# Optimization experiments

Hardware: AMD Instinct MI355X
Metric: run time of the kernel (lower is better)

The kernel has to match this reference:

```python
import jax, jax.numpy as jnp
import numpy as np

COMMITMENT_COST = 0.25


def setup_inputs() -> dict:
    key = jax.random.key(0)
    k1, k2 = jax.random.split(key)
    inputs = jax.random.normal(k1, (16, 1024, 256), dtype=jnp.float32)
    embeddings = jax.random.normal(k2, (8192, 256), dtype=jnp.float32) * 0.1
    return {"inputs": inputs, "embeddings": embeddings}


def reference(inputs, embeddings):
    K, D = embeddings.shape
    input_shape = inputs.shape
    flat = inputs.reshape(-1, D)  # [N, D]
    distances = (
        jnp.sum(flat * flat, axis=1, keepdims=True)
        + jnp.sum(embeddings * embeddings, axis=1)
        - 2.0 * jnp.matmul(flat, embeddings.T)
    )
    encoding_indices = jnp.argmin(distances, axis=1)  # [N]
    # direct codebook gather (same math as one-hot @ embeddings)
    quantized = embeddings[encoding_indices].reshape(input_shape)
    quantized_sg = inputs + jax.lax.stop_gradient(quantized - inputs)
    e_latent_loss = jnp.mean((jax.lax.stop_gradient(quantized) - inputs) ** 2)
    q_latent_loss = jnp.mean((quantized_sg - jax.lax.stop_gradient(quantized)) ** 2)
    loss = q_latent_loss + COMMITMENT_COST * e_latent_loss
    # avg one-hot probabilities = normalized codeword counts
    N = flat.shape[0]
    counts = jnp.zeros((K,), dtype=flat.dtype).at[encoding_indices].add(1.0)
    avg_probs = counts / N
    perplexity = jnp.exp(-jnp.sum(avg_probs * jnp.log(avg_probs + 1e-10)))
    return quantized_sg, encoding_indices, loss, perplexity
```

## Files before the change

### kernel.cpp

```cpp
#include <hip/hip_runtime.h>
#include <math.h>
#include <stdint.h>

#define ND_ROWS 16384
#define DDIM    256
#define KCODES  8192
#define NSEG    128
#define NRG     8

typedef _Float16 f16x4 __attribute__((ext_vector_type(4)));
typedef _Float16 f16x8 __attribute__((ext_vector_type(8)));
typedef float    f32x4v __attribute__((ext_vector_type(4)));
typedef float    f32x16 __attribute__((ext_vector_type(16)));


__device__ __attribute__((always_inline)) inline void load_lds16(const void* g, void* l) {
    __builtin_amdgcn_global_load_lds((const __attribute__((address_space(1))) void*)g,
                                     (__attribute__((address_space(3))) void*)l, 16, 0, 0);
}

__global__ __launch_bounds__(256) void prep_kernel(const float* __restrict__ x,
                                                   const float* __restrict__ emb,
                                                   _Float16* __restrict__ Xp,
                                                   _Float16* __restrict__ Bp,
                                                   float* __restrict__ neF) {
    int wave = (blockIdx.x << 2) + (threadIdx.x >> 6);
    int lane = threadIdx.x & 63;
    if (wave < ND_ROWS) {
        const float* src = x + (size_t)wave * DDIM;
        float4 v = ((const float4*)src)[lane];
        f16x4 hi, lo;
        hi[0] = (_Float16)v.x; lo[0] = (_Float16)(v.x - (float)hi[0]);
        hi[1] = (_Float16)v.y; lo[1] = (_Float16)(v.y - (float)hi[1]);
        hi[2] = (_Float16)v.z; lo[2] = (_Float16)(v.z - (float)hi[2]);
        hi[3] = (_Float16)v.w; lo[3] = (_Float16)(v.w - (float)hi[3]);
        int rb = wave >> 5, rl = wave & 31;
        size_t off = (size_t)rb * 16384 + ((lane >> 2) << 9)
                   + (((lane >> 1) & 1) << 8) + (rl << 3) + ((lane & 1) << 2);
        *(f16x4*)(Xp + off)        = hi;
        *(f16x4*)(Xp + off + 8192) = lo;
    } else {
        int r = wave - ND_ROWS;
        const float* src = emb + (size_t)r * DDIM;
        float4 v = ((const float4*)src)[lane];
        float s = v.x*v.x + v.y*v.y + v.z*v.z + v.w*v.w;
        #pragma unroll
        for (int m = 32; m; m >>= 1) s += __shfl_xor(s, m, 64);
        float4 t;
        t.x = -2.0f * v.x; t.y = -2.0f * v.y; t.z = -2.0f * v.z; t.w = -2.0f * v.w;
        f16x4 hi, lo;
        hi[0] = (_Float16)t.x; lo[0] = (_Float16)(t.x - (float)hi[0]);
        hi[1] = (_Float16)t.y; lo[1] = (_Float16)(t.y - (float)hi[1]);
        hi[2] = (_Float16)t.z; lo[2] = (_Float16)(t.z - (float)hi[2]);
        hi[3] = (_Float16)t.w; lo[3] = (_Float16)(t.w - (float)hi[3]);
        _Float16* dst = Bp + (size_t)r * 512;
        *(f16x4*)(dst + lane * 4)       = hi;
        *(f16x4*)(dst + 256 + lane * 4) = lo;
        if (lane == 0) neF[r] = s;
    }
}

__global__ __launch_bounds__(512, 4) void argmin_seg(
    const _Float16* __restrict__ Xp, const _Float16* __restrict__ Bp,
    const float* __restrict__ neF, unsigned long long* __restrict__ minpair) {
    __shared__ __align__(16) _Float16 Cs[64 * 512];

    const int tid  = threadIdx.x;
    const int lane = tid & 63;
    const int w    = tid >> 6;
    const int c32  = lane & 31;
    const int kg   = lane >> 5;

    const int rg      = blockIdx.x & 7;
    const int seg     = blockIdx.x >> 3;
    const int rowBase = rg * 2048;
    const int code0   = seg * 64;

    #pragma unroll
    for (int i = 0; i < 8; ++i) {
        int cl = w * 8 + i;
        int g  = lane ^ (cl & 7);
        load_lds16((const char*)(Bp + (size_t)(code0 + cl) * 512) + g * 16,
                   (char*)Cs + cl * 1024);
    }
    __syncthreads();

    const int wBase = rowBase + w * 256;
    for (int c2 = 0; c2 < 4; ++c2) {
        const int rb0 = (wBase >> 5) + c2 * 2;
        const char* xb0 = (const char*)Xp + (size_t)rb0 * 32768 + lane * 16;
        const char* xb1 = xb0 + 32768;
        f32x16 acc[2][2];
        #pragma unroll
        for (int i = 0; i < 16; ++i) {
            acc[0][0][i] = 0.0f; acc[0][1][i] = 0.0f;
            acc[1][0][i] = 0.0f; acc[1][1][i] = 0.0f;
        }

        #pragma unroll 2
        for (int q = 0; q < 16; ++q) {
            f16x8 xh0 = *(const f16x8*)(xb0 + q * 1024);
            f16x8 xl0 = *(const f16x8*)(xb0 + 16384 + q * 1024);
            f16x8 xh1 = *(const f16x8*)(xb1 + q * 1024);
            f16x8 xl1 = *(const f16x8*)(xb1 + 16384 + q * 1024);
            f16x8 ch[2], cl2[2];
            #pragma unroll
            for (int mt = 0; mt < 2; ++mt) {
                const char* cp = (const char*)Cs + (mt * 32 + c32) * 1024;
                int ph = (q * 2 + kg) ^ (c32 & 7);
                int pl = (32 + q * 2 + kg) ^ (c32 & 7);
                ch[mt]  = *(const f16x8*)(cp + ph * 16);
                cl2[mt] = *(const f16x8*)(cp + pl * 16);
            }
            acc[0][0] = __builtin_amdgcn_mfma_f32_32x32x16_f16(ch[0],  xh0, acc[0][0], 0, 0, 0);
            acc[0][1] = __builtin_amdgcn_mfma_f32_32x32x16_f16(ch[1],  xh0, acc[0][1], 0, 0, 0);
            acc[1][0] = __builtin_amdgcn_mfma_f32_32x32x16_f16(ch[0],  xh1, acc[1][0], 0, 0, 0);
            acc[1][1] = __builtin_amdgcn_mfma_f32_32x32x16_f16(ch[1],  xh1, acc[1][1], 0, 0, 0);
            acc[0][0] = __builtin_amdgcn_mfma_f32_32x32x16_f16(ch[0],  xl0, acc[0][0], 0, 0, 0);
            acc[0][1] = __builtin_amdgcn_mfma_f32_32x32x16_f16(ch[1],  xl0, acc[0][1], 0, 0, 0);
            acc[1][0] = __builtin_amdgcn_mfma_f32_32x32x16_f16(ch[0],  xl1, acc[1][0], 0, 0, 0);
            acc[1][1] = __builtin_amdgcn_mfma_f32_32x32x16_f16(ch[1],  xl1, acc[1][1], 0, 0, 0);
            acc[0][0] = __builtin_amdgcn_mfma_f32_32x32x16_f16(cl2[0], xh0, acc[0][0], 0, 0, 0);
            acc[0][1] = __builtin_amdgcn_mfma_f32_32x32x16_f16(cl2[1], xh0, acc[0][1], 0, 0, 0);
            acc[1][0] = __builtin_amdgcn_mfma_f32_32x32x16_f16(cl2[0], xh1, acc[1][0], 0, 0, 0);
            acc[1][1] = __builtin_amdgcn_mfma_f32_32x32x16_f16(cl2[1], xh1, acc[1][1], 0, 0, 0);
        }

        f32x4v ne4[2][4];
        #pragma unroll
        for (int mt = 0; mt < 2; ++mt)
            #pragma unroll
            for (int g2 = 0; g2 < 4; ++g2)
                ne4[mt][g2] = *(const f32x4v*)(neF + code0 + mt * 32 + g2 * 8 + 4 * kg);
        #pragma unroll
        for (int ck = 0; ck < 2; ++ck) {
            float best = 3.402823466e+38f;
            int   bi   = 0;
            #pragma unroll
            for (int mt = 0; mt < 2; ++mt)
                #pragma unroll
                for (int r = 0; r < 16; ++r) {
                    float d  = acc[ck][mt][r] + ne4[mt][r >> 2][r & 3];
                    int   id = code0 + mt * 32 + 4 * kg + ((r & 3) + 8 * (r >> 2));
                    if (d < best) { best = d; bi = id; }
                }
            float ov = __shfl_xor(best, 32, 64);
            int   oi = __shfl_xor(bi, 32, 64);
            if (ov < best || (ov == best && oi < bi)) { best = ov; bi = oi; }
            if (kg == 0) {
                int row = (rb0 + ck) * 32 + c32;
                unsigned u = __float_as_uint(best);
                u = (u & 0x80000000u) ? ~u : (u | 0x80000000u);
                atomicMin(&minpair[row],
                          (((unsigned long long)u) << 32) | (unsigned)bi);
            }
        }
    }
}

__global__ __launch_bounds__(256) void finalize_kernel(
    const float* __restrict__ x, const float* __restrict__ emb,
    const unsigned long long* __restrict__ minpair,
    float* __restrict__ out_q, float* __restrict__ out_idx,
    int* __restrict__ counts, float* __restrict__ parts) {
    __shared__ float rde[4], rdq[4];
    int wv   = threadIdx.x >> 6;
    int row  = (blockIdx.x << 2) + wv;
    int lane = threadIdx.x & 63;

    int bi = (int)(minpair[row] & 0xFFFFFFFFull);

    float4 xv = ((const float4*)(x   + (size_t)row * DDIM))[lane];
    float4 ev = ((const float4*)(emb + (size_t)bi  * DDIM))[lane];
    float4 q;
    q.x = xv.x + (ev.x - xv.x);
    q.y = xv.y + (ev.y - xv.y);
    q.z = xv.z + (ev.z - xv.z);
    q.w = xv.w + (ev.w - xv.w);
    ((float4*)(out_q + (size_t)row * DDIM))[lane] = q;

    float de = (ev.x - xv.x) * (ev.x - xv.x) + (ev.y - xv.y) * (ev.y - xv.y)
             + (ev.z - xv.z) * (ev.z - xv.z) + (ev.w - xv.w) * (ev.w - xv.w);
    float dq = (q.x - ev.x) * (q.x - ev.x) + (q.y - ev.y) * (q.y - ev.y)
             + (q.z - ev.z) * (q.z - ev.z) + (q.w - ev.w) * (q.w - ev.w);
    #pragma unroll
    for (int m = 32; m; m >>= 1) {
        de += __shfl_xor(de, m, 64);
        dq += __shfl_xor(dq, m, 64);
    }
    if (lane == 0) {
        out_idx[row] = (float)bi;
        atomicAdd(&counts[bi], 1);
        rde[wv] = de; rdq[wv] = dq;
    }
    __syncthreads();
    if (threadIdx.x == 0) {
        parts[blockIdx.x]        = rde[0] + rde[1] + rde[2] + rde[3];
        parts[4096 + blockIdx.x] = rdq[0] + rdq[1] + rdq[2] + rdq[3];
    }
}

__global__ __launch_bounds__(256) void scalars_kernel(
    const int* __restrict__ counts, const float* __restrict__ parts,
    float* __restrict__ out_loss, float* __restrict__ out_perp) {
    __shared__ float red[256], rde[256], rdq[256];
    float local = 0.0f, de = 0.0f, dq = 0.0f;
    for (int k = threadIdx.x; k < KCODES; k += 256) {
        float p = (float)counts[k] * (1.0f / (float)ND_ROWS);
        local += p * logf(p + 1e-10f);
    }
    for (int k = threadIdx.x; k < 4096; k += 256) {
        de += parts[k];
        dq += parts[4096 + k];
    }
    red[threadIdx.x] = local; rde[threadIdx.x] = de; rdq[threadIdx.x] = dq;
    __syncthreads();
    for (int s = 128; s; s >>= 1) {
        if (threadIdx.x < s) {
            red[threadIdx.x] += red[threadIdx.x + s];
            rde[threadIdx.x] += rde[threadIdx.x + s];
            rdq[threadIdx.x] += rdq[threadIdx.x + s];
        }
        __syncthreads();
    }
    if (threadIdx.x == 0) {
        *out_perp = expf(-red[0]);
        float invn = 1.0f / (float)(ND_ROWS * DDIM);
        *out_loss = rdq[0] * invn + 0.25f * (rde[0] * invn);
    }
}

extern "C" void kernel_launch(void* const* d_in, const int* in_sizes, int n_in,
                              void* d_out, int out_size, void* d_ws, size_t ws_size,
                              hipStream_t stream) {
    const float* x   = (const float*)d_in[0];
    const float* emb = (const float*)d_in[1];

    char* ws = (char*)d_ws;
    unsigned long long* minpair = (unsigned long long*)ws;
    int*      counts = (int*)(ws + 131072);
    float*    parts  = (float*)(ws + 163840);
    float*    neF    = (float*)(ws + 196608);
    _Float16* Xp     = (_Float16*)(ws + 229376);
    _Float16* Bp     = (_Float16*)(ws + 17006592);

    float* out_q    = (float*)d_out;
    float* out_idx  = out_q + (size_t)ND_ROWS * DDIM;
    float* out_loss = out_idx + ND_ROWS;
    float* out_perp = out_loss + 1;

    hipMemsetAsync(minpair, 0xFF, ND_ROWS * sizeof(unsigned long long), stream);
    hipMemsetAsync(counts, 0, KCODES * sizeof(int), stream);

    prep_kernel<<<(KCODES + ND_ROWS) / 4, 256, 0, stream>>>(x, emb, Xp, Bp, neF);
    argmin_seg<<<NRG * NSEG, 512, 0, stream>>>(Xp, Bp, neF, minpair);
    finalize_kernel<<<ND_ROWS / 4, 256, 0, stream>>>(x, emb, minpair,
                                                     out_q, out_idx, counts, parts);
    scalars_kernel<<<1, 256, 0, stream>>>(counts, parts, out_loss, out_perp);
}
```

Before: 311.9 us.

## Widen per-wave row tile to four blocks with double-buffered register loads

Each wave now processes 4 row-blocks of 32 (128 rows) per group instead of 2, so each codebook fragment read from LDS feeds twice as many MFMAs. Loads for the next k-step are software-pipelined into a second register stage, and s_setprio is raised around the MFMA bursts. Occupancy is reduced to 2 blocks per CU to leave room for the larger accumulator and staging registers, which risks less latency hiding and register spills.

```diff
diff --git a/kernel.cpp b/kernel.cpp
--- a/kernel.cpp
+++ b/kernel.cpp
@@ -60,7 +60,59 @@
     }
 }
 
-__global__ __launch_bounds__(512, 4) void argmin_seg(
+#define MFMA16(A, B, C) __builtin_amdgcn_mfma_f32_32x32x16_f16(A, B, C, 0, 0, 0)
+
+#define DECL_STAGE(P) f16x8 P##xh0, P##xh1, P##xh2, P##xh3, \
+                            P##xl0, P##xl1, P##xl2, P##xl3, \
+                            P##c0, P##c1, P##d0, P##d1;
+
+#define LOADX(P, qq) { \
+    P##xh0 = *(const f16x8*)(xb + (qq) * 1024); \
+    P##xl0 = *(const f16x8*)(xb + 16384 + (qq) * 1024); \
+    P##xh1 = *(const f16x8*)(xb + 32768 + (qq) * 1024); \
+    P##xl1 = *(const f16x8*)(xb + 32768 + 16384 + (qq) * 1024); \
+    P##xh2 = *(const f16x8*)(xb + 65536 + (qq) * 1024); \
+    P##xl2 = *(const f16x8*)(xb + 65536 + 16384 + (qq) * 1024); \
+    P##xh3 = *(const f16x8*)(xb + 98304 + (qq) * 1024); \
+    P##xl3 = *(const f16x8*)(xb + 98304 + 16384 + (qq) * 1024); }
+
+#define LOADC(P, qq) { \
+    const int ph_ = (((qq) * 2 + kg) ^ sw); \
+    const int pl_ = ((32 + (qq) * 2 + kg) ^ sw); \
+    P##c0 = *(const f16x8*)(cp0 + ph_ * 16); \
+    P##c1 = *(const f16x8*)(cp1 + ph_ * 16); \
+    P##d0 = *(const f16x8*)(cp0 + pl_ * 16); \
+    P##d1 = *(const f16x8*)(cp1 + pl_ * 16); }
+
+#define MFMAS(P) \
+    __builtin_amdgcn_s_setprio(1); \
+    acc[0][0] = MFMA16(P##c0, P##xh0, acc[0][0]); \
+    acc[0][1] = MFMA16(P##c1, P##xh0, acc[0][1]); \
+    acc[1][0] = MFMA16(P##c0, P##xh1, acc[1][0]); \
+    acc[1][1] = MFMA16(P##c1, P##xh1, acc[1][1]); \
+    acc[2][0] = MFMA16(P##c0, P##xh2, acc[2][0]); \
+    acc[2][1] = MFMA16(P##c1, P##xh2, acc[2][1]); \
+    acc[3][0] = MFMA16(P##c0, P##xh3, acc[3][0]); \
+    acc[3][1] = MFMA16(P##c1, P##xh3, acc[3][1]); \
+    acc[0][0] = MFMA16(P##c0, P##xl0, acc[0][0]); \
+    acc[0][1] = MFMA16(P##c1, P##xl0, acc[0][1]); \
+    acc[1][0] = MFMA16(P##c0, P##xl1, acc[1][0]); \
+    acc[1][1] = MFMA16(P##c1, P##xl1, acc[1][1]); \
+    acc[2][0] = MFMA16(P##c0, P##xl2, acc[2][0]); \
+    acc[2][1] = MFMA16(P##c1, P##xl2, acc[2][1]); \
+    acc[3][0] = MFMA16(P##c0, P##xl3, acc[3][0]); \
+    acc[3][1] = MFMA16(P##c1, P##xl3, acc[3][1]); \
+    acc[0][0] = MFMA16(P##d0, P##xh0, acc[0][0]); \
+    acc[0][1] = MFMA16(P##d1, P##xh0, acc[0][1]); \
+    acc[1][0] = MFMA16(P##d0, P##xh1, acc[1][0]); \
+    acc[1][1] = MFMA16(P##d1, P##xh1, acc[1][1]); \
+    acc[2][0] = MFMA16(P##d0, P##xh2, acc[2][0]); \
+    acc[2][1] = MFMA16(P##d1, P##xh2, acc[2][1]); \
+    acc[3][0] = MFMA16(P##d0, P##xh3, acc[3][0]); \
+    acc[3][1] = MFMA16(P##d1, P##xh3, acc[3][1]); \
+    __builtin_amdgcn_s_setprio(0);
+
+__global__ __launch_bounds__(512, 2) void argmin_seg(
     const _Float16* __restrict__ Xp, const _Float16* __restrict__ Bp,
     const float* __restrict__ neF, unsigned long long* __restrict__ minpair) {
     __shared__ __align__(16) _Float16 Cs[64 * 512];
@@ -70,6 +122,7 @@
     const int w    = tid >> 6;
     const int c32  = lane & 31;
     const int kg   = lane >> 5;
+    const int sw   = c32 & 7;
 
     const int rg      = blockIdx.x & 7;
     const int seg     = blockIdx.x >> 3;
@@ -85,45 +138,36 @@
     }
     __syncthreads();
 
+    const char* cp0 = (const char*)Cs + c32 * 1024;
+    const char* cp1 = cp0 + 32768;
+
     const int wBase = rowBase + w * 256;
-    for (int c2 = 0; c2 < 4; ++c2) {
-        const int rb0 = (wBase >> 5) + c2 * 2;
-        const char* xb0 = (const char*)Xp + (size_t)rb0 * 32768 + lane * 16;
-        const char* xb1 = xb0 + 32768;
-        f32x16 acc[2][2];
-        #pragma unroll
-        for (int i = 0; i < 16; ++i) {
-            acc[0][0][i] = 0.0f; acc[0][1][i] = 0.0f;
-            acc[1][0][i] = 0.0f; acc[1][1][i] = 0.0f;
+    #pragma unroll 1
+    for (int grp = 0; grp < 2; ++grp) {
+        const int rb0 = (wBase >> 5) + grp * 4;
+        const char* xb = (const char*)Xp + (size_t)rb0 * 32768 + lane * 16;
+
+        f32x16 acc[4][2];
+        #pragma unroll
+        for (int ck = 0; ck < 4; ++ck) {
+            #pragma unroll
+            for (int i = 0; i < 16; ++i) { acc[ck][0][i] = 0.0f; acc[ck][1][i] = 0.0f; }
         }
 
-        #pragma unroll 2
-        for (int q = 0; q < 16; ++q) {
-            f16x8 xh0 = *(const f16x8*)(xb0 + q * 1024);
-            f16x8 xl0 = *(const f16x8*)(xb0 + 16384 + q * 1024);
-            f16x8 xh1 = *(const f16x8*)(xb1 + q * 1024);
-            f16x8 xl1 = *(const f16x8*)(xb1 + 16384 + q * 1024);
-            f16x8 ch[2], cl2[2];
-            #pragma unroll
-            for (int mt = 0; mt < 2; ++mt) {
-                const char* cp = (const char*)Cs + (mt * 32 + c32) * 1024;
-                int ph = (q * 2 + kg) ^ (c32 & 7);
-                int pl = (32 + q * 2 + kg) ^ (c32 & 7);
-                ch[mt]  = *(const f16x8*)(cp + ph * 16);
-                cl2[mt] = *(const f16x8*)(cp + pl * 16);
+        DECL_STAGE(a)
+        DECL_STAGE(b)
+        LOADX(a, 0)
+        LOADC(a, 0)
+        #pragma unroll
+        for (int q = 0; q < 16; q += 2) {
+            LOADX(b, q + 1)
+            LOADC(b, q + 1)
+            MFMAS(a)
+            if (q + 2 < 16) {
+                LOADX(a, q + 2)
+                LOADC(a, q + 2)
             }
-            acc[0][0] = __builtin_amdgcn_mfma_f32_32x32x16_f16(ch[0],  xh0, acc[0][0], 0, 0, 0);
-            acc[0][1] = __builtin_amdgcn_mfma_f32_32x32x16_f16(ch[1],  xh0, acc[0][1], 0, 0, 0);
-            acc[1][0] = __builtin_amdgcn_mfma_f32_32x32x16_f16(ch[0],  xh1, acc[1][0], 0, 0, 0);
-            acc[1][1] = __builtin_amdgcn_mfma_f32_32x32x16_f16(ch[1],  xh1, acc[1][1], 0, 0, 0);
-            acc[0][0] = __builtin_amdgcn_mfma_f32_32x32x16_f16(ch[0],  xl0, acc[0][0], 0, 0, 0);
-            acc[0][1] = __builtin_amdgcn_mfma_f32_32x32x16_f16(ch[1],  xl0, acc[0][1], 0, 0, 0);
-            acc[1][0] = __builtin_amdgcn_mfma_f32_32x32x16_f16(ch[0],  xl1, acc[1][0], 0, 0, 0);
-            acc[1][1] = __builtin_amdgcn_mfma_f32_32x32x16_f16(ch[1],  xl1, acc[1][1], 0, 0, 0);
-            acc[0][0] = __builtin_amdgcn_mfma_f32_32x32x16_f16(cl2[0], xh0, acc[0][0], 0, 0, 0);
-            acc[0][1] = __builtin_amdgcn_mfma_f32_32x32x16_f16(cl2[1], xh0, acc[0][1], 0, 0, 0);
-            acc[1][0] = __builtin_amdgcn_mfma_f32_32x32x16_f16(cl2[0], xh1, acc[1][0], 0, 0, 0);
-            acc[1][1] = __builtin_amdgcn_mfma_f32_32x32x16_f16(cl2[1], xh1, acc[1][1], 0, 0, 0);
+            MFMAS(b)
         }
 
         f32x4v ne4[2][4];
@@ -133,7 +177,7 @@
             for (int g2 = 0; g2 < 4; ++g2)
                 ne4[mt][g2] = *(const f32x4v*)(neF + code0 + mt * 32 + g2 * 8 + 4 * kg);
         #pragma unroll
-        for (int ck = 0; ck < 2; ++ck) {
+        for (int ck = 0; ck < 4; ++ck) {
             float best = 3.402823466e+38f;
             int   bi   = 0;
             #pragma unroll
```

Result: slower. 550.6 us (+76.6%).
